# Optimization experiments

Hardware: AMD Instinct MI355X
Metric: run time of the kernel (lower is better)

Reference implementation:

```python
import jax, jax.numpy as jnp
import numpy as np

NQ, NT, D = 2048, 131072, 64   # query nodes, target nodes, feature dim
E = 2_000_000                  # candidate (u, v) edges
M = 1024                       # consensus (nn_map) pairs; vc = top M rows of Xt


def setup_inputs() -> dict:
    key = jax.random.key(0)
    ks = jax.random.split(key, 8)
    Xq = jax.random.normal(ks[0], (NQ, D), dtype=jnp.float32)
    Xt = jax.random.normal(ks[1], (NT, D), dtype=jnp.float32)
    W_alpha = jax.random.normal(ks[2], (D, D), dtype=jnp.float32) * 0.05
    b_alpha = jax.random.normal(ks[3], (1,), dtype=jnp.float32) * 0.05
    W_beta = jax.random.normal(ks[4], (D, D), dtype=jnp.float32) * 0.05
    b_beta = jax.random.normal(ks[5], (1,), dtype=jnp.float32) * 0.05
    u_idx = jax.random.randint(ks[6], (E,), 0, NQ, dtype=jnp.int32)
    # candidate targets live in [0, NT - M); consensus targets in [NT - M, NT)
    v_idx = jax.random.randint(ks[7], (E,), 0, NT - M, dtype=jnp.int32)
    uc = jax.random.randint(jax.random.fold_in(key, 7), (M,), 0, NQ, dtype=jnp.int32)
    vc = (NT - M) + jnp.arange(M, dtype=jnp.int32)
    return {"Xq": Xq, "Xt": Xt, "W_alpha": W_alpha, "b_alpha": b_alpha,
            "W_beta": W_beta, "b_beta": b_beta,
            "u_idx": u_idx, "v_idx": v_idx, "uc": uc, "vc": vc}


def reference(Xq, Xt, W_alpha, b_alpha, W_beta, b_beta, u_idx, v_idx, uc, vc):
    # 1) consensus overwrite: Xt[vc] = Xq[uc]  (nn_map)
    Xt_c = Xt.at[vc].set(Xq[uc])

    # 2) per-edge gather + bilinear interaction scoring
    xq_e = Xq[u_idx]      # [E, D]
    xt_e = Xt_c[v_idx]    # [E, D]

    def bilinear(W, b):
        return jnp.einsum('ed,df,ef->e', xq_e, W, xt_e) + b[0]

    beta = jax.nn.sigmoid(bilinear(W_beta, b_beta))   # [E] gate
    alpha = jax.nn.elu(bilinear(W_alpha, b_alpha))    # [E] score
    h_e = (1.0 - beta)[:, None] * xq_e + beta[:, None] * xt_e  # [E, D]

    # 3) segment softmax over incoming u per target v (== masked softmax over Nq)
    m = jax.ops.segment_max(alpha, v_idx, num_segments=NT)     # -inf on empty segments
    a = jnp.exp(alpha - m[v_idx])
    s = jax.ops.segment_sum(a, v_idx, num_segments=NT)
    a = a / s[v_idx] + 1e-10   # matches original +1e-10 after normalization

    # 4) scatter-aggregate weighted messages back into Xt rows with >=1 candidate
    agg = jax.ops.segment_sum(a[:, None] * h_e, v_idx, num_segments=NT)  # [NT, D]
    deg = jax.ops.segment_sum(jnp.ones_like(alpha), v_idx, num_segments=NT)
    Xt_out = jnp.where((deg > 0)[:, None], agg, Xt_c)
    return (Xq, Xt_out)
```

## Files before the change

kernel.cpp:

```cpp
#include <hip/hip_runtime.h>

#define NQ 2048
#define NT 131072
#define DD 64
#define MM 1024
#define NBUCK 512
#define BCAP 4608
#define CHUNK 4096


typedef __attribute__((ext_vector_type(2))) _Float16 h2;

#if defined(__has_builtin)
#if __has_builtin(__builtin_amdgcn_fdot2)
#define HAVE_FDOT2 1
#endif
#endif

__device__ __forceinline__ float fdot2(h2 a, h2 b, float c) {
#ifdef HAVE_FDOT2
    return __builtin_amdgcn_fdot2(a, b, c, false);
#else
    return fmaf((float)a.x, (float)b.x, fmaf((float)a.y, (float)b.y, c));
#endif
}

__global__ __launch_bounds__(1024) void bin_yq_kernel(
        const int* __restrict__ u_idx, const int* __restrict__ v_idx,
        int* __restrict__ gcurP, unsigned* __restrict__ gbuf,
        const float* __restrict__ Xq,
        const float* __restrict__ Wa, const float* __restrict__ Wb,
        _Float16* __restrict__ YX16,
        float* __restrict__ outXq, int E) {
    __shared__ unsigned stage[CHUNK];
    __shared__ int hist[NBUCK], off[NBUCK], base[NBUCK], cur[NBUCK];
    int tid = threadIdx.x;
    int nchunks = (E + CHUNK - 1) / CHUNK;

    if (blockIdx.x >= nchunks) {
        int r = (blockIdx.x - nchunks) * 16 + (tid >> 6);
        int j = tid & 63;
        float sa = 0.f, sb = 0.f;
#pragma unroll
        for (int k = 0; k < DD; ++k) {
            float x = Xq[r * DD + k];
            sa = fmaf(x, Wa[k * DD + j], sa);
            sb = fmaf(x, Wb[k * DD + j], sb);
        }
        int rb = r << 8;
        int gbase = rb + (j >> 2) * 8 + (j & 3);
        YX16[gbase] = (_Float16)sa;
        YX16[gbase + 4] = (_Float16)sb;
        float xj = Xq[r * DD + j];
        YX16[rb + 128 + j] = (_Float16)xj;
        YX16[rb + 192 + j] = (_Float16)0.f;
        outXq[r * DD + j] = xj;
        return;
    }

    int e0 = blockIdx.x * CHUNK;
    int n = min(CHUNK, E - e0);
    if (n <= 0) return;

    for (int i = tid; i < NBUCK; i += 1024) hist[i] = 0;
    __syncthreads();

    unsigned p[4];
    int nv = 0;
    int i0 = tid * 4;
    if (i0 + 3 < n) {
        int4 u4 = *(const int4*)(u_idx + e0 + i0);
        int4 v4 = *(const int4*)(v_idx + e0 + i0);
        p[0] = ((unsigned)v4.x << 11) | (unsigned)u4.x;
        p[1] = ((unsigned)v4.y << 11) | (unsigned)u4.y;
        p[2] = ((unsigned)v4.z << 11) | (unsigned)u4.z;
        p[3] = ((unsigned)v4.w << 11) | (unsigned)u4.w;
        nv = 4;
    } else {
        for (int j = 0; j < 4; ++j) {
            if (i0 + j < n) {
                p[j] = ((unsigned)v_idx[e0 + i0 + j] << 11) | (unsigned)u_idx[e0 + i0 + j];
                ++nv;
            }
        }
    }
    for (int j = 0; j < nv; ++j) atomicAdd(&hist[p[j] >> 19], 1);
    __syncthreads();
    if (tid < 64) {
        int h[8], sum = 0;
#pragma unroll
        for (int j = 0; j < 8; ++j) { h[j] = hist[8 * tid + j]; sum += h[j]; }
        int incl = sum;
#pragma unroll
        for (int d = 1; d < 64; d <<= 1) {
            int y = __shfl_up(incl, d, 64);
            if (tid >= d) incl += y;
        }
        int excl = incl - sum;
#pragma unroll
        for (int j = 0; j < 8; ++j) { off[8 * tid + j] = excl; excl += h[j]; }
    }
    __syncthreads();
    for (int i = tid; i < NBUCK; i += 1024) {
        base[i] = hist[i] ? atomicAdd(&gcurP[i << 4], hist[i]) : 0;
        cur[i] = off[i];
    }
    __syncthreads();
    for (int j = 0; j < nv; ++j) {
        int pos = atomicAdd(&cur[p[j] >> 19], 1);
        stage[pos] = p[j];
    }
    __syncthreads();
    for (int i = tid; i < n; i += 1024) {
        unsigned q = stage[i];
        int b = q >> 19;
        int idx = base[b] + (i - off[b]);
        if (idx < BCAP) gbuf[(size_t)b * BCAP + idx] = q;
    }
}

__global__ __launch_bounds__(1024, 2) void bucket_sort_kernel(
        const int* __restrict__ gcurP,
        unsigned* __restrict__ gbuf,
        int* __restrict__ rofsg) {
    __shared__ unsigned short su[BCAP];
    __shared__ int hist[256], cur[256], rstart[257];
    int tid = threadIdx.x;
    int b = blockIdx.x;
    int n = min(gcurP[b << 4], BCAP);

    if (tid < 256) hist[tid] = 0;
    __syncthreads();
    for (int i = tid; i < n; i += 1024)
        atomicAdd(&hist[(gbuf[(size_t)b * BCAP + i] >> 11) & 255], 1);
    __syncthreads();
    if (tid < 64) {
        int h0 = hist[4 * tid], h1 = hist[4 * tid + 1];
        int h2_ = hist[4 * tid + 2], h3 = hist[4 * tid + 3];
        int tot = h0 + h1 + h2_ + h3;
        int incl = tot;
#pragma unroll
        for (int d = 1; d < 64; d <<= 1) {
            int y = __shfl_up(incl, d, 64);
            if (tid >= d) incl += y;
        }
        int excl = incl - tot;
        rstart[4 * tid] = excl;             cur[4 * tid] = excl;
        rstart[4 * tid + 1] = excl + h0;    cur[4 * tid + 1] = excl + h0;
        rstart[4 * tid + 2] = excl + h0 + h1;       cur[4 * tid + 2] = excl + h0 + h1;
        rstart[4 * tid + 3] = excl + h0 + h1 + h2_; cur[4 * tid + 3] = excl + h0 + h1 + h2_;
        if (tid == 63) rstart[256] = excl + tot;
    }
    __syncthreads();
    for (int i = tid; i < n; i += 1024) {
        unsigned p = gbuf[(size_t)b * BCAP + i];
        int pos = atomicAdd(&cur[(p >> 11) & 255], 1);
        su[pos] = (unsigned short)(p & 0x7FFu);
    }
    __syncthreads();
    unsigned* dst = gbuf + (size_t)b * BCAP;
    int nw = (n + 1) >> 1;
    for (int i = tid; i < nw; i += 1024)
        dst[i] = ((const unsigned*)su)[i];
    if (tid <= 256) rofsg[b * 257 + tid] = rstart[tid];
}

template <int CTRL>
__device__ __forceinline__ float dpp_add(float x) {
    int xi = __builtin_bit_cast(int, x);
    int yi = __builtin_amdgcn_update_dpp(xi, xi, CTRL, 0xF, 0xF, true);
    return x + __builtin_bit_cast(float, yi);
}
__device__ __forceinline__ float red16(float x) {
    x = dpp_add<0xB1>(x);
    x = dpp_add<0x4E>(x);
    x = dpp_add<0x124>(x);
    x = dpp_add<0x128>(x);
    return x;
}

__global__ __launch_bounds__(1024, 2) void row_kernel(
        const float* __restrict__ Xq,
        const float* __restrict__ Xt,
        const _Float16* __restrict__ YX16,
        const float* __restrict__ ba,
        const float* __restrict__ bb,
        const unsigned* __restrict__ gbuf,
        const int* __restrict__ rofsg,
        const int* __restrict__ uc,
        float* __restrict__ outXt) {
    __shared__ unsigned short su[BCAP];
    __shared__ int rstart[257];
    int tid = threadIdx.x;
    int b = blockIdx.x;

    if (tid <= 256) rstart[tid] = rofsg[b * 257 + tid];
    __syncthreads();
    int n = rstart[256];
    int nw = (n + 1) >> 1;
    const unsigned* src = gbuf + (size_t)b * BCAP;
    for (int i = tid; i < nw; i += 1024)
        ((unsigned*)su)[i] = src[i];
    __syncthreads();

    int lane = tid & 63;
    int w = tid >> 6;
    int l16 = lane & 15;
    int g = lane >> 4;
    float ba0 = ba[0], bb0 = bb[0];

    for (int r = w; r < 256; r += 16) {
        int v = (b << 8) + r;
        int startr = rstart[r];
        int deg = rstart[r + 1] - startr;
        if (deg == 0) {
            if (g == 0) {
                float4 o;
                if (v >= NT - MM) {
                    int u = uc[v - (NT - MM)];
                    o = ((const float4*)(Xq + (size_t)u * DD))[l16];
                } else {
                    o = ((const float4*)(Xt + (size_t)v * DD))[l16];
                }
                ((float4*)(outXt + (size_t)v * DD))[l16] = o;
            }
            continue;
        }
        float4 xt4 = ((const float4*)(Xt + (size_t)v * DD))[l16];
        h2 xt01, xt23;
        xt01.x = (_Float16)xt4.x; xt01.y = (_Float16)xt4.y;
        xt23.x = (_Float16)xt4.z; xt23.y = (_Float16)xt4.w;
        float4 acc = make_float4(0.f, 0.f, 0.f, 0.f);
        float s = 0.f;
        float s2 = 0.f;
        for (int base = 0; base < deg; base += 8) {
            int e0 = base + g;
            int e1 = base + 4 + g;
            bool ok0 = e0 < deg, ok1 = e1 < deg;
            int u0 = (int)su[startr + (ok0 ? e0 : 0)];
            int u1 = (int)su[startr + (ok1 ? e1 : 0)];
            const _Float16* P0 = YX16 + ((size_t)u0 << 8);
            const _Float16* P1 = YX16 + ((size_t)u1 << 8);
            float4 y0 = *(const float4*)(P0 + (l16 << 3));
            float4 y1 = *(const float4*)(P1 + (l16 << 3));
            float2 xv0 = *(const float2*)(P0 + 128 + (l16 << 2));
            float2 xv1 = *(const float2*)(P1 + 128 + (l16 << 2));
            float pa0 = fdot2(__builtin_bit_cast(h2, y0.y), xt23,
                       fdot2(__builtin_bit_cast(h2, y0.x), xt01, 0.f));
            float pb0 = fdot2(__builtin_bit_cast(h2, y0.w), xt23,
                       fdot2(__builtin_bit_cast(h2, y0.z), xt01, 0.f));
            float pa1 = fdot2(__builtin_bit_cast(h2, y1.y), xt23,
                       fdot2(__builtin_bit_cast(h2, y1.x), xt01, 0.f));
            float pb1 = fdot2(__builtin_bit_cast(h2, y1.w), xt23,
                       fdot2(__builtin_bit_cast(h2, y1.z), xt01, 0.f));
            pa0 = red16(pa0); pb0 = red16(pb0);
            pa1 = red16(pa1); pb1 = red16(pb1);
            float la0 = pa0 + ba0, la1 = pa1 + ba0;
            float t0 = __expf(la0), t1 = __expf(la1);
            float al0 = la0 > 0.f ? la0 : (t0 - 1.f);
            float al1 = la1 > 0.f ? la1 : (t1 - 1.f);
            float a0 = ok0 ? __expf(al0) : 0.f;
            float a1 = ok1 ? __expf(al1) : 0.f;
            float be0 = __builtin_amdgcn_rcpf(1.f + __expf(-(pb0 + bb0)));
            float be1 = __builtin_amdgcn_rcpf(1.f + __expf(-(pb1 + bb0)));
            float c20 = a0 * be0, c21 = a1 * be1;
            float c10 = a0 - c20, c11 = a1 - c21;
            h2 q0a = __builtin_bit_cast(h2, xv0.x), q0b = __builtin_bit_cast(h2, xv0.y);
            h2 q1a = __builtin_bit_cast(h2, xv1.x), q1b = __builtin_bit_cast(h2, xv1.y);
            acc.x = fmaf((float)q0a.x, c10, acc.x);
            acc.y = fmaf((float)q0a.y, c10, acc.y);
            acc.z = fmaf((float)q0b.x, c10, acc.z);
            acc.w = fmaf((float)q0b.y, c10, acc.w);
            acc.x = fmaf((float)q1a.x, c11, acc.x);
            acc.y = fmaf((float)q1a.y, c11, acc.y);
            acc.z = fmaf((float)q1b.x, c11, acc.z);
            acc.w = fmaf((float)q1b.y, c11, acc.w);
            s += a0 + a1;
            s2 += c20 + c21;
        }
        acc.x += __shfl_xor(acc.x, 16, 64);
        acc.y += __shfl_xor(acc.y, 16, 64);
        acc.z += __shfl_xor(acc.z, 16, 64);
        acc.w += __shfl_xor(acc.w, 16, 64);
        s     += __shfl_xor(s, 16, 64);
        s2    += __shfl_xor(s2, 16, 64);
        acc.x += __shfl_xor(acc.x, 32, 64);
        acc.y += __shfl_xor(acc.y, 32, 64);
        acc.z += __shfl_xor(acc.z, 32, 64);
        acc.w += __shfl_xor(acc.w, 32, 64);
        s     += __shfl_xor(s, 32, 64);
        s2    += __shfl_xor(s2, 32, 64);
        if (g == 0) {
            float inv = __builtin_amdgcn_rcpf(s);
            float4 o;
            o.x = fmaf(s2, xt4.x, acc.x) * inv;
            o.y = fmaf(s2, xt4.y, acc.y) * inv;
            o.z = fmaf(s2, xt4.z, acc.z) * inv;
            o.w = fmaf(s2, xt4.w, acc.w) * inv;
            ((float4*)(outXt + (size_t)v * DD))[l16] = o;
        }
    }
}

extern "C" void kernel_launch(void* const* d_in, const int* in_sizes, int n_in,
                              void* d_out, int out_size, void* d_ws, size_t ws_size,
                              hipStream_t stream) {
    const float* Xq = (const float*)d_in[0];
    const float* Xt = (const float*)d_in[1];
    const float* Wa = (const float*)d_in[2];
    const float* ba = (const float*)d_in[3];
    const float* Wb = (const float*)d_in[4];
    const float* bb = (const float*)d_in[5];
    const int* u_idx = (const int*)d_in[6];
    const int* v_idx = (const int*)d_in[7];
    const int* uc = (const int*)d_in[8];
    const int* vc = (const int*)d_in[9];
    const int E = in_sizes[6];
    (void)vc;

    float* out = (float*)d_out;
    float* outXq = out;
    float* outXt = out + NQ * DD;

    char* ws = (char*)d_ws;
    _Float16* YX16 = (_Float16*)ws;   ws += (size_t)NQ * 256 * sizeof(_Float16);
    int* gcurP = (int*)ws;            ws += (size_t)NBUCK * 16 * sizeof(int);
    int* rofsg = (int*)ws;            ws += (size_t)NBUCK * 257 * sizeof(int);
    ws = (char*)(((size_t)ws + 255) & ~(size_t)255);
    unsigned* gbuf = (unsigned*)ws;   ws += (size_t)NBUCK * BCAP * sizeof(unsigned);

    hipMemsetAsync(gcurP, 0, (size_t)NBUCK * 16 * sizeof(int), stream);

    int nchunks = (E + CHUNK - 1) / CHUNK;
    bin_yq_kernel<<<nchunks + NQ / 16, 1024, 0, stream>>>(
        u_idx, v_idx, gcurP, gbuf, Xq, Wa, Wb, YX16, outXq, E);

    bucket_sort_kernel<<<NBUCK, 1024, 0, stream>>>(gcurP, gbuf, rofsg);

    row_kernel<<<NBUCK, 1024, 0, stream>>>(Xq, Xt, YX16, ba, bb, gbuf, rofsg,
                                           uc, outXt);
}
```

Baseline: 215.6 us.

## Fuse bucket sort into row kernel and widen per-lane feature slice to 8 lanes

```diff
diff --git a/kernel.cpp b/kernel.cpp
--- a/kernel.cpp
+++ b/kernel.cpp
@@ -48,9 +48,9 @@
             sb = fmaf(x, Wb[k * DD + j], sb);
         }
         int rb = r << 8;
-        int gbase = rb + (j >> 2) * 8 + (j & 3);
+        int gbase = rb + ((j >> 3) << 4) + (j & 7);
         YX16[gbase] = (_Float16)sa;
-        YX16[gbase + 4] = (_Float16)sb;
+        YX16[gbase + 8] = (_Float16)sb;
         float xj = Xq[r * DD + j];
         YX16[rb + 128 + j] = (_Float16)xj;
         YX16[rb + 192 + j] = (_Float16)0.f;
@@ -119,10 +119,29 @@
     }
 }
 
-__global__ __launch_bounds__(1024, 2) void bucket_sort_kernel(
+template <int CTRL>
+__device__ __forceinline__ float dpp_add(float x) {
+    int xi = __builtin_bit_cast(int, x);
+    int yi = __builtin_amdgcn_update_dpp(xi, xi, CTRL, 0xF, 0xF, true);
+    return x + __builtin_bit_cast(float, yi);
+}
+__device__ __forceinline__ float red8(float x) {
+    x = dpp_add<0xB1>(x);
+    x = dpp_add<0x4E>(x);
+    x = dpp_add<0x141>(x);
+    return x;
+}
+
+__global__ __launch_bounds__(1024, 2) void bucket_kernel(
+        const float* __restrict__ Xq,
+        const float* __restrict__ Xt,
+        const _Float16* __restrict__ YX16,
+        const float* __restrict__ ba,
+        const float* __restrict__ bb,
         const int* __restrict__ gcurP,
-        unsigned* __restrict__ gbuf,
-        int* __restrict__ rofsg) {
+        const unsigned* __restrict__ gbuf,
+        const int* __restrict__ uc,
+        float* __restrict__ outXt) {
     __shared__ unsigned short su[BCAP];
     __shared__ int hist[256], cur[256], rstart[257];
     int tid = threadIdx.x;
@@ -158,55 +177,11 @@
         su[pos] = (unsigned short)(p & 0x7FFu);
     }
     __syncthreads();
-    unsigned* dst = gbuf + (size_t)b * BCAP;
-    int nw = (n + 1) >> 1;
-    for (int i = tid; i < nw; i += 1024)
-        dst[i] = ((const unsigned*)su)[i];
-    if (tid <= 256) rofsg[b * 257 + tid] = rstart[tid];
-}
-
-template <int CTRL>
-__device__ __forceinline__ float dpp_add(float x) {
-    int xi = __builtin_bit_cast(int, x);
-    int yi = __builtin_amdgcn_update_dpp(xi, xi, CTRL, 0xF, 0xF, true);
-    return x + __builtin_bit_cast(float, yi);
-}
-__device__ __forceinline__ float red16(float x) {
-    x = dpp_add<0xB1>(x);
-    x = dpp_add<0x4E>(x);
-    x = dpp_add<0x124>(x);
-    x = dpp_add<0x128>(x);
-    return x;
-}
-
-__global__ __launch_bounds__(1024, 2) void row_kernel(
-        const float* __restrict__ Xq,
-        const float* __restrict__ Xt,
-        const _Float16* __restrict__ YX16,
-        const float* __restrict__ ba,
-        const float* __restrict__ bb,
-        const unsigned* __restrict__ gbuf,
-        const int* __restrict__ rofsg,
-        const int* __restrict__ uc,
-        float* __restrict__ outXt) {
-    __shared__ unsigned short su[BCAP];
-    __shared__ int rstart[257];
-    int tid = threadIdx.x;
-    int b = blockIdx.x;
-
-    if (tid <= 256) rstart[tid] = rofsg[b * 257 + tid];
-    __syncthreads();
-    int n = rstart[256];
-    int nw = (n + 1) >> 1;
-    const unsigned* src = gbuf + (size_t)b * BCAP;
-    for (int i = tid; i < nw; i += 1024)
-        ((unsigned*)su)[i] = src[i];
-    __syncthreads();
 
     int lane = tid & 63;
     int w = tid >> 6;
-    int l16 = lane & 15;
-    int g = lane >> 4;
+    int l8 = lane & 7;
+    int g8 = lane >> 3;
     float ba0 = ba[0], bb0 = bb[0];
 
     for (int r = w; r < 256; r += 16) {
@@ -214,47 +189,61 @@
         int startr = rstart[r];
         int deg = rstart[r + 1] - startr;
         if (deg == 0) {
-            if (g == 0) {
-                float4 o;
+            if (lane < 8) {
+                const float4* srcp;
                 if (v >= NT - MM) {
-                    int u = uc[v - (NT - MM)];
-                    o = ((const float4*)(Xq + (size_t)u * DD))[l16];
+                    srcp = (const float4*)(Xq + (size_t)uc[v - (NT - MM)] * DD);
                 } else {
-                    o = ((const float4*)(Xt + (size_t)v * DD))[l16];
+                    srcp = (const float4*)(Xt + (size_t)v * DD);
                 }
-                ((float4*)(outXt + (size_t)v * DD))[l16] = o;
+                float4 o0 = srcp[lane * 2];
+                float4 o1 = srcp[lane * 2 + 1];
+                ((float4*)(outXt + (size_t)v * DD))[lane * 2] = o0;
+                ((float4*)(outXt + (size_t)v * DD))[lane * 2 + 1] = o1;
             }
             continue;
         }
-        float4 xt4 = ((const float4*)(Xt + (size_t)v * DD))[l16];
-        h2 xt01, xt23;
-        xt01.x = (_Float16)xt4.x; xt01.y = (_Float16)xt4.y;
-        xt23.x = (_Float16)xt4.z; xt23.y = (_Float16)xt4.w;
-        float4 acc = make_float4(0.f, 0.f, 0.f, 0.f);
+        float4 xtA = ((const float4*)(Xt + (size_t)v * DD))[l8 * 2];
+        float4 xtB = ((const float4*)(Xt + (size_t)v * DD))[l8 * 2 + 1];
+        h2 xh0, xh1, xh2, xh3;
+        xh0.x = (_Float16)xtA.x; xh0.y = (_Float16)xtA.y;
+        xh1.x = (_Float16)xtA.z; xh1.y = (_Float16)xtA.w;
+        xh2.x = (_Float16)xtB.x; xh2.y = (_Float16)xtB.y;
+        xh3.x = (_Float16)xtB.z; xh3.y = (_Float16)xtB.w;
+        float4 accA = make_float4(0.f, 0.f, 0.f, 0.f);
+        float4 accB = make_float4(0.f, 0.f, 0.f, 0.f);
         float s = 0.f;
         float s2 = 0.f;
-        for (int base = 0; base < deg; base += 8) {
-            int e0 = base + g;
-            int e1 = base + 4 + g;
+        for (int base = 0; base < deg; base += 16) {
+            int e0 = base + g8;
+            int e1 = base + 8 + g8;
             bool ok0 = e0 < deg, ok1 = e1 < deg;
             int u0 = (int)su[startr + (ok0 ? e0 : 0)];
             int u1 = (int)su[startr + (ok1 ? e1 : 0)];
             const _Float16* P0 = YX16 + ((size_t)u0 << 8);
             const _Float16* P1 = YX16 + ((size_t)u1 << 8);
-            float4 y0 = *(const float4*)(P0 + (l16 << 3));
-            float4 y1 = *(const float4*)(P1 + (l16 << 3));
-            float2 xv0 = *(const float2*)(P0 + 128 + (l16 << 2));
-            float2 xv1 = *(const float2*)(P1 + 128 + (l16 << 2));
-            float pa0 = fdot2(__builtin_bit_cast(h2, y0.y), xt23,
-                       fdot2(__builtin_bit_cast(h2, y0.x), xt01, 0.f));
-            float pb0 = fdot2(__builtin_bit_cast(h2, y0.w), xt23,
-                       fdot2(__builtin_bit_cast(h2, y0.z), xt01, 0.f));
-            float pa1 = fdot2(__builtin_bit_cast(h2, y1.y), xt23,
-                       fdot2(__builtin_bit_cast(h2, y1.x), xt01, 0.f));
-            float pb1 = fdot2(__builtin_bit_cast(h2, y1.w), xt23,
-                       fdot2(__builtin_bit_cast(h2, y1.z), xt01, 0.f));
-            pa0 = red16(pa0); pb0 = red16(pb0);
-            pa1 = red16(pa1); pb1 = red16(pb1);
+            float4 ya0 = *(const float4*)(P0 + (l8 << 4));
+            float4 yb0 = *(const float4*)(P0 + (l8 << 4) + 8);
+            float4 ya1 = *(const float4*)(P1 + (l8 << 4));
+            float4 yb1 = *(const float4*)(P1 + (l8 << 4) + 8);
+            float pa0 = fdot2(__builtin_bit_cast(h2, ya0.w), xh3,
+                       fdot2(__builtin_bit_cast(h2, ya0.z), xh2,
+                       fdot2(__builtin_bit_cast(h2, ya0.y), xh1,
+                       fdot2(__builtin_bit_cast(h2, ya0.x), xh0, 0.f))));
+            float pb0 = fdot2(__builtin_bit_cast(h2, yb0.w), xh3,
+                       fdot2(__builtin_bit_cast(h2, yb0.z), xh2,
+                       fdot2(__builtin_bit_cast(h2, yb0.y), xh1,
+                       fdot2(__builtin_bit_cast(h2, yb0.x), xh0, 0.f))));
+            float pa1 = fdot2(__builtin_bit_cast(h2, ya1.w), xh3,
+                       fdot2(__builtin_bit_cast(h2, ya1.z), xh2,
+                       fdot2(__builtin_bit_cast(h2, ya1.y), xh1,
+                       fdot2(__builtin_bit_cast(h2, ya1.x), xh0, 0.f))));
+            float pb1 = fdot2(__builtin_bit_cast(h2, yb1.w), xh3,
+                       fdot2(__builtin_bit_cast(h2, yb1.z), xh2,
+                       fdot2(__builtin_bit_cast(h2, yb1.y), xh1,
+                       fdot2(__builtin_bit_cast(h2, yb1.x), xh0, 0.f))));
+            pa0 = red8(pa0); pb0 = red8(pb0);
+            pa1 = red8(pa1); pb1 = red8(pb1);
             float la0 = pa0 + ba0, la1 = pa1 + ba0;
             float t0 = __expf(la0), t1 = __expf(la1);
             float al0 = la0 > 0.f ? la0 : (t0 - 1.f);
@@ -265,39 +254,57 @@
             float be1 = __builtin_amdgcn_rcpf(1.f + __expf(-(pb1 + bb0)));
             float c20 = a0 * be0, c21 = a1 * be1;
             float c10 = a0 - c20, c11 = a1 - c21;
-            h2 q0a = __builtin_bit_cast(h2, xv0.x), q0b = __builtin_bit_cast(h2, xv0.y);
-            h2 q1a = __builtin_bit_cast(h2, xv1.x), q1b = __builtin_bit_cast(h2, xv1.y);
-            acc.x = fmaf((float)q0a.x, c10, acc.x);
-            acc.y = fmaf((float)q0a.y, c10, acc.y);
-            acc.z = fmaf((float)q0b.x, c10, acc.z);
-            acc.w = fmaf((float)q0b.y, c10, acc.w);
-            acc.x = fmaf((float)q1a.x, c11, acc.x);
-            acc.y = fmaf((float)q1a.y, c11, acc.y);
-            acc.z = fmaf((float)q1b.x, c11, acc.z);
-            acc.w = fmaf((float)q1b.y, c11, acc.w);
+            float4 xv0 = *(const float4*)(P0 + 128 + (l8 << 3));
+            float4 xv1 = *(const float4*)(P1 + 128 + (l8 << 3));
+            h2 q00 = __builtin_bit_cast(h2, xv0.x), q01 = __builtin_bit_cast(h2, xv0.y);
+            h2 q02 = __builtin_bit_cast(h2, xv0.z), q03 = __builtin_bit_cast(h2, xv0.w);
+            h2 q10 = __builtin_bit_cast(h2, xv1.x), q11 = __builtin_bit_cast(h2, xv1.y);
+            h2 q12 = __builtin_bit_cast(h2, xv1.z), q13 = __builtin_bit_cast(h2, xv1.w);
+            accA.x = fmaf((float)q00.x, c10, accA.x);
+            accA.y = fmaf((float)q00.y, c10, accA.y);
+            accA.z = fmaf((float)q01.x, c10, accA.z);
+            accA.w = fmaf((float)q01.y, c10, accA.w);
+            accB.x = fmaf((float)q02.x, c10, accB.x);
+            accB.y = fmaf((float)q02.y, c10, accB.y);
+            accB.z = fmaf((float)q03.x, c10, accB.z);
+            accB.w = fmaf((float)q03.y, c10, accB.w);
+            accA.x = fmaf((float)q10.x, c11, accA.x);
+            accA.y = fmaf((float)q10.y, c11, accA.y);
+            accA.z = fmaf((float)q11.x, c11, accA.z);
+            accA.w = fmaf((float)q11.y, c11, accA.w);
+            accB.x = fmaf((float)q12.x, c11, accB.x);
+            accB.y = fmaf((float)q12.y, c11, accB.y);
+            accB.z = fmaf((float)q13.x, c11, accB.z);
+            accB.w = fmaf((float)q13.y, c11, accB.w);
             s += a0 + a1;
             s2 += c20 + c21;
         }
-        acc.x += __shfl_xor(acc.x, 16, 64);
-        acc.y += __shfl_xor(acc.y, 16, 64);
-        acc.z += __shfl_xor(acc.z, 16, 64);
-        acc.w += __shfl_xor(acc.w, 16, 64);
-        s     += __shfl_xor(s, 16, 64);
-        s2    += __shfl_xor(s2, 16, 64);
-        acc.x += __shfl_xor(acc.x, 32, 64);
-        acc.y += __shfl_xor(acc.y, 32, 64);
-        acc.z += __shfl_xor(acc.z, 32, 64);
-        acc.w += __shfl_xor(acc.w, 32, 64);
-        s     += __shfl_xor(s, 32, 64);
-        s2    += __shfl_xor(s2, 32, 64);
-        if (g == 0) {
+#pragma unroll
+        for (int offr = 8; offr <= 32; offr <<= 1) {
+            accA.x += __shfl_xor(accA.x, offr, 64);
+            accA.y += __shfl_xor(accA.y, offr, 64);
+            accA.z += __shfl_xor(accA.z, offr, 64);
+            accA.w += __shfl_xor(accA.w, offr, 64);
+            accB.x += __shfl_xor(accB.x, offr, 64);
+            accB.y += __shfl_xor(accB.y, offr, 64);
+            accB.z += __shfl_xor(accB.z, offr, 64);
+            accB.w += __shfl_xor(accB.w, offr, 64);
+            s      += __shfl_xor(s, offr, 64);
+            s2     += __shfl_xor(s2, offr, 64);
+        }
+        if (lane < 8) {
             float inv = __builtin_amdgcn_rcpf(s);
-            float4 o;
-            o.x = fmaf(s2, xt4.x, acc.x) * inv;
-            o.y = fmaf(s2, xt4.y, acc.y) * inv;
-            o.z = fmaf(s2, xt4.z, acc.z) * inv;
-            o.w = fmaf(s2, xt4.w, acc.w) * inv;
-            ((float4*)(outXt + (size_t)v * DD))[l16] = o;
+            float4 oA, oB;
+            oA.x = fmaf(s2, xtA.x, accA.x) * inv;
+            oA.y = fmaf(s2, xtA.y, accA.y) * inv;
+            oA.z = fmaf(s2, xtA.z, accA.z) * inv;
+            oA.w = fmaf(s2, xtA.w, accA.w) * inv;
+            oB.x = fmaf(s2, xtB.x, accB.x) * inv;
+            oB.y = fmaf(s2, xtB.y, accB.y) * inv;
+            oB.z = fmaf(s2, xtB.z, accB.z) * inv;
+            oB.w = fmaf(s2, xtB.w, accB.w) * inv;
+            ((float4*)(outXt + (size_t)v * DD))[lane * 2] = oA;
+            ((float4*)(outXt + (size_t)v * DD))[lane * 2 + 1] = oB;
         }
     }
 }
@@ -325,7 +332,6 @@
     char* ws = (char*)d_ws;
     _Float16* YX16 = (_Float16*)ws;   ws += (size_t)NQ * 256 * sizeof(_Float16);
     int* gcurP = (int*)ws;            ws += (size_t)NBUCK * 16 * sizeof(int);
-    int* rofsg = (int*)ws;            ws += (size_t)NBUCK * 257 * sizeof(int);
     ws = (char*)(((size_t)ws + 255) & ~(size_t)255);
     unsigned* gbuf = (unsigned*)ws;   ws += (size_t)NBUCK * BCAP * sizeof(unsigned);
 
@@ -335,8 +341,6 @@
     bin_yq_kernel<<<nchunks + NQ / 16, 1024, 0, stream>>>(
         u_idx, v_idx, gcurP, gbuf, Xq, Wa, Wb, YX16, outXq, E);
 
-    bucket_sort_kernel<<<NBUCK, 1024, 0, stream>>>(gcurP, gbuf, rofsg);
-
-    row_kernel<<<NBUCK, 1024, 0, stream>>>(Xq, Xt, YX16, ba, bb, gbuf, rofsg,
-                                           uc, outXt);
-}
+    bucket_kernel<<<NBUCK, 1024, 0, stream>>>(Xq, Xt, YX16, ba, bb, gcurP, gbuf,
+                                              uc, outXt);
+}
```

Result: no change. 218.3 us (+1.3%).
